# Performance work log

Hardware: AMD Instinct MI355X
Metric: run time of the kernel (lower is better)

The kernel has to match this reference:

```python
import math
import jax, jax.numpy as jnp
import numpy as np

B, T, C, H = 2, 2048, 1024, 16
D = C // H


def _slopes(n):
    def p2(m):
        start = 2 ** (-(2 ** -(math.log2(m) - 3)))
        return [start * start ** i for i in range(m)]
    if math.log2(n).is_integer():
        return p2(n)
    c = 2 ** math.floor(math.log2(n))
    return p2(c) + _slopes(2 * c)[0::2][: n - c]


def setup_inputs() -> dict:
    key = jax.random.key(0)
    ks = jax.random.split(key, 9)
    std = 0.02
    x = jax.random.normal(ks[0], (B, T, C), dtype=jnp.float32)
    Wq = std * jax.random.normal(ks[1], (C, C), dtype=jnp.float32)
    Wk = std * jax.random.normal(ks[2], (C, C), dtype=jnp.float32)
    Wv = std * jax.random.normal(ks[3], (C, C), dtype=jnp.float32)
    # fc_resid init: std 0.02/sqrt(num_layers)
    Wo = (std / math.sqrt(24.0)) * jax.random.normal(ks[4], (C, C), dtype=jnp.float32)
    bq = jnp.zeros((C,), jnp.float32)
    bk = jnp.zeros((C,), jnp.float32)
    bv = jnp.zeros((C,), jnp.float32)
    bo = jnp.zeros((C,), jnp.float32)
    return {"x": x, "Wq": Wq, "bq": bq, "Wk": Wk, "bk": bk,
            "Wv": Wv, "bv": bv, "Wo": Wo, "bo": bo}


def reference(x, Wq, bq, Wk, bk, Wv, bv, Wo, bo):
    # projections -> [B, T, H, D]
    q = (x @ Wq + bq).reshape(B, T, H, D)
    k = (x @ Wk + bk).reshape(B, T, H, D)
    v = (x @ Wv + bv).reshape(B, T, H, D)

    scale = 1.0 / math.sqrt(D)
    att = jnp.einsum("bqhd,bkhd->bhqk", q, k) * scale  # [B,H,T,T]

    slopes = jnp.asarray(_slopes(H), dtype=jnp.float32)  # [H]
    i = jnp.arange(T)
    rel = i[None, :] - i[None, :].T  # rel[i,j] = j - i
    causal = rel <= 0  # j <= i
    # alibi bias: -tril(i - j) = tril(j - i), scaled per head
    alibi = slopes[:, None, None] * jnp.where(causal, rel, 0).astype(jnp.float32)

    att = att + alibi[None]  # broadcast over batch
    att = jnp.where(causal[None, None], att, -jnp.inf)
    att = jax.nn.softmax(att, axis=-1)

    y = jnp.einsum("bhqk,bkhd->bqhd", att, v).reshape(B, T, C)
    return y @ Wo + bo  # dropout p=0 (eval) is identity
```

## Files before the change

### kernel.cpp

```cpp
#include <hip/hip_runtime.h>
#include <hip/hip_bf16.h>

typedef __bf16 bf16;
typedef __bf16 bf16x4 __attribute__((ext_vector_type(4)));
typedef __bf16 bf16x8 __attribute__((ext_vector_type(8)));
typedef float floatx4 __attribute__((ext_vector_type(4)));

#define B_ 2
#define T_ 2048
#define C_ 1024
#define H_ 16
#define D_ 64
#define M_ 4096
#define QK_LD 2048

__device__ __forceinline__ void load_lds16(const void* g, void* l) {
  __builtin_amdgcn_global_load_lds(
      (const __attribute__((address_space(1))) unsigned int*)g,
      (__attribute__((address_space(3))) unsigned int*)l, 16, 0, 0);
}

struct PrepArgs { const float* w[4]; bf16* wt[4]; const float* x; bf16* xb; };

__global__ __launch_bounds__(256)
void prep(PrepArgs p) {
  const int bid = blockIdx.x;
  if (bid < 4096) {
    __shared__ float tile[32][33];
    const int z = bid >> 10, xy = bid & 1023;
    const int bx = xy & 31, by = xy >> 5;
    const float* in = p.w[z];
    bf16* out = p.wt[z];
    int tx = threadIdx.x & 31, ty = threadIdx.x >> 5;
    int n0 = bx * 32, k0 = by * 32;
#pragma unroll
    for (int j = 0; j < 32; j += 8)
      tile[ty + j][tx] = in[(size_t)(k0 + ty + j) * C_ + n0 + tx];
    __syncthreads();
#pragma unroll
    for (int j = 0; j < 32; j += 8)
      out[(size_t)(n0 + ty + j) * C_ + k0 + tx] = (bf16)tile[tx][ty + j];
  } else {
    int i = ((bid - 4096) * 256 + threadIdx.x) * 8;
    float4 a = *(const float4*)(p.x + i);
    float4 b = *(const float4*)(p.x + i + 4);
    bf16x8 o;
    o[0] = (bf16)a.x; o[1] = (bf16)a.y; o[2] = (bf16)a.z; o[3] = (bf16)a.w;
    o[4] = (bf16)b.x; o[5] = (bf16)b.y; o[6] = (bf16)b.z; o[7] = (bf16)b.w;
    *(bf16x8*)(p.xb + i) = o;
  }
}

struct GQ {
  const bf16* A; const bf16* Bt;
  const float* bias[3];
  bf16* Cout; bf16* vt; int N; int K;
};

__global__ __launch_bounds__(256, 2)
void gemm128(GQ g) {
  __shared__ __align__(16) bf16 As[128 * 64];
  __shared__ __align__(16) bf16 Bs[128 * 64];
  const int tid = threadIdx.x;
  const int wave = tid >> 6, lane = tid & 63;
  const int quad = lane >> 4, l16 = lane & 15;
  const int m0 = blockIdx.y * 128, n0 = blockIdx.x * 128;
  const int wm = (wave >> 1) * 64, wn = (wave & 1) * 64;

  floatx4 acc[4][4] = {};

  int rA[4], cA[4];
#pragma unroll
  for (int t = 0; t < 4; ++t) {
    int pch = (wave * 4 + t) * 64 + lane;
    rA[t] = pch >> 3;
    cA[t] = (pch & 7) ^ (rA[t] & 7);
  }

  for (int k0 = 0; k0 < g.K; k0 += 64) {
    __syncthreads();
#pragma unroll
    for (int t = 0; t < 4; ++t) {
      load_lds16(g.A + (size_t)(m0 + rA[t]) * g.K + k0 + cA[t] * 8,
                 As + (wave * 4 + t) * 512);
      load_lds16(g.Bt + (size_t)(n0 + rA[t]) * g.K + k0 + cA[t] * 8,
                 Bs + (wave * 4 + t) * 512);
    }
    __builtin_amdgcn_s_waitcnt(0x0f70);
    __syncthreads();
#pragma unroll
    for (int s = 0; s < 2; ++s) {
      bf16x8 af[4], bfr[4];
#pragma unroll
      for (int i = 0; i < 4; ++i) {
        int mr = wm + i * 16 + l16;
        af[i] = *(const bf16x8*)(As + ((mr * 8) + ((s * 4 + quad) ^ (mr & 7))) * 8);
        int nr = wn + i * 16 + l16;
        bfr[i] = *(const bf16x8*)(Bs + ((nr * 8) + ((s * 4 + quad) ^ (nr & 7))) * 8);
      }
#pragma unroll
      for (int i = 0; i < 4; ++i)
#pragma unroll
        for (int j = 0; j < 4; ++j)
          acc[i][j] = __builtin_amdgcn_mfma_f32_16x16x32_bf16(af[i], bfr[j],
                                                              acc[i][j], 0, 0, 0);
    }
  }

  const bool vsplit = (n0 >= 2048);
#pragma unroll
  for (int j = 0; j < 4; ++j) {
    int col = n0 + wn + j * 16 + l16;
    const float* bp = g.bias[col >> 10];
    float bv = bp[col & 1023];
    if (vsplit) {
      int cv = col - 2048;
      bf16* dst0 = g.vt + ((size_t)((m0 >> 11) * 16 + (cv >> 6)) * 64 + (cv & 63)) * (size_t)T_
                   + (m0 & 2047) + wm + quad * 4;
#pragma unroll
      for (int i = 0; i < 4; ++i) {
        bf16x4 pk;
#pragma unroll
        for (int r = 0; r < 4; ++r) pk[r] = (bf16)(acc[i][j][r] + bv);
        *(bf16x4*)(dst0 + i * 16) = pk;
      }
    } else {
#pragma unroll
      for (int i = 0; i < 4; ++i) {
#pragma unroll
        for (int r = 0; r < 4; ++r) {
          int row = m0 + wm + i * 16 + quad * 4 + r;
          g.Cout[(size_t)row * g.N + col] = (bf16)(acc[i][j][r] + bv);
        }
      }
    }
  }
}

__global__ __launch_bounds__(256, 2)
void gemm_out(const bf16* __restrict__ A, const bf16* __restrict__ Bt,
              const float* __restrict__ bias, float* __restrict__ C) {
  __shared__ __align__(16) bf16 As[64 * 64];
  __shared__ __align__(16) bf16 Bs[128 * 64];
  const int tid = threadIdx.x;
  const int wave = tid >> 6, lane = tid & 63;
  const int quad = lane >> 4, l16 = lane & 15;
  const int m0 = blockIdx.y * 64, n0 = blockIdx.x * 128;
  const int wm = (wave >> 1) * 32, wn = (wave & 1) * 64;

  floatx4 acc[2][4] = {};

  int rA[2], cA[2], rB[4], cB[4];
#pragma unroll
  for (int t = 0; t < 2; ++t) {
    int p = t * 256 + tid;
    rA[t] = p >> 3; cA[t] = (p & 7) ^ (rA[t] & 7);
  }
#pragma unroll
  for (int t = 0; t < 4; ++t) {
    int p = t * 256 + tid;
    rB[t] = p >> 3; cB[t] = (p & 7) ^ (rB[t] & 7);
  }

  for (int k0 = 0; k0 < 1024; k0 += 64) {
    __syncthreads();
#pragma unroll
    for (int t = 0; t < 2; ++t)
      load_lds16(A + (size_t)(m0 + rA[t]) * 1024 + k0 + cA[t] * 8,
                 As + t * 2048 + wave * 512);
#pragma unroll
    for (int t = 0; t < 4; ++t)
      load_lds16(Bt + (size_t)(n0 + rB[t]) * 1024 + k0 + cB[t] * 8,
                 Bs + t * 2048 + wave * 512);
    __builtin_amdgcn_s_waitcnt(0x0f70);
    __syncthreads();
#pragma unroll
    for (int s = 0; s < 2; ++s) {
      bf16x8 af[2], bfr[4];
#pragma unroll
      for (int i = 0; i < 2; ++i) {
        int mr = wm + i * 16 + l16;
        af[i] = *(const bf16x8*)(As + ((mr * 8) + ((s * 4 + quad) ^ (mr & 7))) * 8);
      }
#pragma unroll
      for (int j = 0; j < 4; ++j) {
        int nr = wn + j * 16 + l16;
        bfr[j] = *(const bf16x8*)(Bs + ((nr * 8) + ((s * 4 + quad) ^ (nr & 7))) * 8);
      }
#pragma unroll
      for (int i = 0; i < 2; ++i)
#pragma unroll
        for (int j = 0; j < 4; ++j)
          acc[i][j] = __builtin_amdgcn_mfma_f32_16x16x32_bf16(af[i], bfr[j],
                                                              acc[i][j], 0, 0, 0);
    }
  }

#pragma unroll
  for (int j = 0; j < 4; ++j) {
    int col = n0 + wn + j * 16 + l16;
    float bv = bias[col];
#pragma unroll
    for (int i = 0; i < 2; ++i)
#pragma unroll
      for (int r = 0; r < 4; ++r) {
        int row = m0 + wm + i * 16 + quad * 4 + r;
        C[(size_t)row * 1024 + col] = acc[i][j][r] + bv;
      }
  }
}

__constant__ int yy_map[24] = {7, 8, 16, 9, 17, 6, 10, 18, 11, 19, 5, 12,
                               20, 13, 21, 4, 14, 22, 15, 23, 3, 2, 1, 0};

__global__ __launch_bounds__(512, 2)
void attn8(const bf16* __restrict__ qk, const bf16* __restrict__ vt,
           bf16* __restrict__ y, bf16* __restrict__ po, float* __restrict__ pl) {
  __shared__ __align__(16) bf16 smem[8192 + 8192 + 8 * 576];
  const int tid = threadIdx.x, wave = tid >> 6, lane = tid & 63;
  const int quad = lane >> 4, l16 = lane & 15;
  const int qs = wave >> 1, kh = wave & 1;
  const int bh = blockIdx.x, b = bh >> 4, h = bh & 15;
  const int yy = yy_map[blockIdx.y];
  int qb, kbeg, kcnt, seg;
  if (yy < 8)       { qb = yy;      kbeg = 0;      kcnt = 2 * qb + 2; seg = -1; }
  else if (yy < 16) { qb = 23 - yy; kbeg = 0;      kcnt = qb + 1;     seg = 0;  }
  else              { qb = 31 - yy; kbeg = qb + 1; kcnt = qb + 1;     seg = 1;  }

  const float L2E = 1.4426950408889634f;
  const float slope2 = exp2f(-0.5f * (float)(h + 1)) * L2E;
  const float scl2 = 0.125f * L2E;
  const float M0 = 14.0f;

  bf16x8 ones;
  {
    bf16 v1 = (l16 == 0) ? (bf16)1.0f : (bf16)0.0f;
#pragma unroll
    for (int j = 0; j < 8; ++j) ones[j] = v1;
  }

  const int rS = tid >> 3;
  const int cS = (tid & 7) ^ (rS & 7);
  const bf16* kbase = qk + (size_t)b * T_ * QK_LD + 1024 + h * 64;
  const bf16* vbase = vt + (size_t)bh * 64 * T_;

  bf16* Plw = smem + 16384 + wave * 576;
  const int q0 = qb * 128;
  const int w0 = q0 + qs * 32;

  bf16x8 qf[2][2];
  float rowoff[2][4];
#pragma unroll
  for (int qt = 0; qt < 2; ++qt) {
#pragma unroll
    for (int s = 0; s < 2; ++s)
      qf[qt][s] = *(const bf16x8*)(qk +
          (size_t)(b * T_ + w0 + qt * 16 + l16) * QK_LD + h * 64 + s * 32 + quad * 8);
#pragma unroll
    for (int r = 0; r < 4; ++r)
      rowoff[qt][r] = slope2 * (float)(w0 + qt * 16 + quad * 4 + r) + M0;
  }

  floatx4 o[2][5];
#pragma unroll
  for (int qt = 0; qt < 2; ++qt)
#pragma unroll
    for (int n = 0; n < 5; ++n) o[qt][n] = (floatx4)0.f;

  load_lds16(kbase + (size_t)(kbeg * 64 + rS) * QK_LD + cS * 8, smem + wave * 512);
  load_lds16(vbase + (size_t)rS * T_ + kbeg * 64 + cS * 8, smem + 8192 + wave * 512);
  __builtin_amdgcn_s_waitcnt(0x0f70);
  __syncthreads();

  for (int it = 0; it < kcnt; ++it) {
    const int kj0 = (kbeg + it) * 64;
    const int cur = it & 1;

    if (it + 1 < kcnt) {
      const int nk = kj0 + 64;
      load_lds16(kbase + (size_t)(nk + rS) * QK_LD + cS * 8,
                 smem + (cur ^ 1) * 4096 + wave * 512);
      load_lds16(vbase + (size_t)rS * T_ + nk + cS * 8,
                 smem + 8192 + (cur ^ 1) * 4096 + wave * 512);
    }

    const bf16* Klc = smem + cur * 4096;
    const bf16* Vlc = smem + 8192 + cur * 4096;
    bf16x8 kf[2][2], vf[4];
#pragma unroll
    for (int ss = 0; ss < 2; ++ss)
#pragma unroll
      for (int kt = 0; kt < 2; ++kt) {
        const int krow = kh * 32 + kt * 16 + l16;
        kf[ss][kt] = *(const bf16x8*)(Klc + krow * 64 +
                                      (((ss * 4 + quad) ^ (krow & 7)) * 8));
      }
#pragma unroll
    for (int nt = 0; nt < 4; ++nt) {
      const int drow = nt * 16 + l16;
      vf[nt] = *(const bf16x8*)(Vlc + drow * 64 +
                                (((kh * 4 + quad) ^ (drow & 7)) * 8));
    }

    float scol[2];
#pragma unroll
    for (int kt = 0; kt < 2; ++kt)
      scol[kt] = slope2 * (float)(kj0 + kh * 32 + kt * 16 + l16);

#pragma unroll
    for (int qt = 0; qt < 2; ++qt) {
      const int rb = w0 + qt * 16;
      floatx4 sa[2] = {};
#pragma unroll
      for (int ss = 0; ss < 2; ++ss)
#pragma unroll
        for (int kt = 0; kt < 2; ++kt)
          sa[kt] = __builtin_amdgcn_mfma_f32_16x16x32_bf16(qf[qt][ss], kf[ss][kt],
                                                           sa[kt], 0, 0, 0);

      if (kj0 + kh * 32 + 31 > rb) {
#pragma unroll
        for (int kt = 0; kt < 2; ++kt)
#pragma unroll
          for (int r = 0; r < 4; ++r) {
            const int row = rb + quad * 4 + r;
            float p = __builtin_amdgcn_exp2f(
                fmaf(sa[kt][r], scl2, scol[kt]) - rowoff[qt][r]);
            if (kj0 + kh * 32 + kt * 16 + l16 > row) p = 0.f;
            Plw[(quad * 4 + r) * 36 + kt * 16 + l16] = (bf16)p;
          }
      } else {
#pragma unroll
        for (int kt = 0; kt < 2; ++kt)
#pragma unroll
          for (int r = 0; r < 4; ++r)
            Plw[(quad * 4 + r) * 36 + kt * 16 + l16] = (bf16)__builtin_amdgcn_exp2f(
                fmaf(sa[kt][r], scl2, scol[kt]) - rowoff[qt][r]);
      }

      __builtin_amdgcn_s_waitcnt(0xc07f);

      bf16x8 pf = *(const bf16x8*)(Plw + l16 * 36 + quad * 8);
#pragma unroll
      for (int nt = 0; nt < 4; ++nt)
        o[qt][nt] = __builtin_amdgcn_mfma_f32_16x16x32_bf16(pf, vf[nt],
                                                            o[qt][nt], 0, 0, 0);
      o[qt][4] = __builtin_amdgcn_mfma_f32_16x16x32_bf16(pf, ones, o[qt][4], 0, 0, 0);
    }

    __builtin_amdgcn_s_waitcnt(0x0f70);
    __syncthreads();
  }

  float* Cb = (float*)smem;
  if (kh == 1) {
#pragma unroll
    for (int qt = 0; qt < 2; ++qt)
#pragma unroll
      for (int n = 0; n < 5; ++n)
        *(floatx4*)(Cb + (((qs * 2 + qt) * 5 + n) * 64 + lane) * 4) = o[qt][n];
  }
  __syncthreads();
  if (kh == 1) return;
#pragma unroll
  for (int qt = 0; qt < 2; ++qt)
#pragma unroll
    for (int n = 0; n < 5; ++n)
      o[qt][n] += *(const floatx4*)(Cb + (((qs * 2 + qt) * 5 + n) * 64 + lane) * 4);

  if (seg < 0) {
#pragma unroll
    for (int qt = 0; qt < 2; ++qt)
#pragma unroll
      for (int r = 0; r < 4; ++r) {
        float lsum = __shfl(o[qt][4][r], lane & 48);
        float inv = 1.f / lsum;
        const int row = w0 + qt * 16 + quad * 4 + r;
#pragma unroll
        for (int nt = 0; nt < 4; ++nt)
          y[(size_t)(b * T_ + row) * C_ + h * 64 + nt * 16 + l16] =
              (bf16)(o[qt][nt][r] * inv);
      }
  } else {
    const int pid = (bh * 8 + (qb - 8)) * 2 + seg;
    bf16* pob = po + (size_t)pid * 8192;
#pragma unroll
    for (int qt = 0; qt < 2; ++qt) {
#pragma unroll
      for (int half = 0; half < 2; ++half) {
        bf16x8 pk;
#pragma unroll
        for (int jj = 0; jj < 8; ++jj) {
          int j = half * 8 + jj;
          pk[jj] = (bf16)o[qt][j >> 2][j & 3];
        }
        *(bf16x8*)(pob + (qt * 2 + half) * 2048 + (qs * 64 + lane) * 8) = pk;
      }
#pragma unroll
      for (int r = 0; r < 4; ++r)
        if (l16 == 0)
          pl[pid * 128 + qs * 32 + qt * 16 + quad * 4 + r] = o[qt][4][r];
    }
  }
}

__global__ __launch_bounds__(256)
void combine(const bf16* __restrict__ po, const float* __restrict__ pl,
             bf16* __restrict__ y) {
  const int x = blockIdx.x;
  const int bh = x >> 3, qb = (x & 7) + 8;
  const int b = bh >> 4, h = bh & 15;
  const int pid0 = (bh * 8 + (qb - 8)) * 2;
  const bf16* p0 = po + (size_t)pid0 * 8192;
  const bf16* p1 = p0 + 8192;
  const int t = threadIdx.x;
  const int wave = t >> 6, quad = (t >> 4) & 3, l16 = t & 15;

  float linv[2][4];
#pragma unroll
  for (int qt = 0; qt < 2; ++qt)
#pragma unroll
    for (int r = 0; r < 4; ++r) {
      const int row = wave * 32 + qt * 16 + quad * 4 + r;
      linv[qt][r] = 1.f / (pl[pid0 * 128 + row] + pl[(pid0 + 1) * 128 + row]);
    }

#pragma unroll
  for (int qt = 0; qt < 2; ++qt)
#pragma unroll
    for (int half = 0; half < 2; ++half) {
      bf16x8 a = *(const bf16x8*)(p0 + (qt * 2 + half) * 2048 + t * 8);
      bf16x8 c = *(const bf16x8*)(p1 + (qt * 2 + half) * 2048 + t * 8);
#pragma unroll
      for (int jj = 0; jj < 8; ++jj) {
        int j = half * 8 + jj;
        const int nt = j >> 2, r = j & 3;
        const int row = wave * 32 + qt * 16 + quad * 4 + r;
        const int col = nt * 16 + l16;
        float v = ((float)a[jj] + (float)c[jj]) * linv[qt][r];
        y[(size_t)(b * T_ + qb * 128 + row) * C_ + h * 64 + col] = (bf16)v;
      }
    }
}

extern "C" void kernel_launch(void* const* d_in, const int* in_sizes, int n_in,
                              void* d_out, int out_size, void* d_ws, size_t ws_size,
                              hipStream_t stream) {
  const float* x  = (const float*)d_in[0];
  const float* Wq = (const float*)d_in[1];
  const float* bq = (const float*)d_in[2];
  const float* Wk = (const float*)d_in[3];
  const float* bk = (const float*)d_in[4];
  const float* Wv = (const float*)d_in[5];
  const float* bv = (const float*)d_in[6];
  const float* Wo = (const float*)d_in[7];
  const float* bo = (const float*)d_in[8];

  bf16* ws  = (bf16*)d_ws;
  bf16* WtQ = ws;
  bf16* WtK = WtQ + (size_t)C_ * C_;
  bf16* WtV = WtK + (size_t)C_ * C_;
  bf16* WtO = WtV + (size_t)C_ * C_;
  bf16* xb  = WtO + (size_t)C_ * C_;
  bf16* qkb = xb + (size_t)M_ * C_;
  bf16* vtb = qkb + (size_t)M_ * 2 * C_;
  bf16* yb  = vtb + (size_t)M_ * C_;
  bf16* pob = yb + (size_t)M_ * C_;
  float* plb = (float*)(pob + (size_t)512 * 8192);

  PrepArgs pp;
  pp.w[0] = Wq; pp.w[1] = Wk; pp.w[2] = Wv; pp.w[3] = Wo;
  pp.wt[0] = WtQ; pp.wt[1] = WtK; pp.wt[2] = WtV; pp.wt[3] = WtO;
  pp.x = x; pp.xb = xb;
  prep<<<dim3(4096 + M_ * C_ / (256 * 8)), 256, 0, stream>>>(pp);

  GQ gq;
  gq.A = xb; gq.Bt = WtQ;
  gq.bias[0] = bq; gq.bias[1] = bk; gq.bias[2] = bv;
  gq.Cout = qkb; gq.vt = vtb; gq.N = 2 * C_; gq.K = C_;
  gemm128<<<dim3(24, 32), 256, 0, stream>>>(gq);

  attn8<<<dim3(32, 24), 512, 0, stream>>>(qkb, vtb, yb, pob, plb);
  combine<<<dim3(32 * 8), 256, 0, stream>>>(pob, plb, yb);

  gemm_out<<<dim3(8, 64), 256, 0, stream>>>(yb, WtO, bo, (float*)d_out);
}
```

Before: 189.1 us.

## Compute transposed scores to keep P in registers and drop LDS round-trip

Attention now computes S^T = K·Q^T, so each lane's MFMA output can be fed directly as the B operand of 16x16x16 MFMAs for P·V. This removes the per-wave LDS staging of P, its wait, and the extra 'ones' MFMA used for row sums. Row sums are instead accumulated in registers and reduced with shuffles. Output stores become vectorized bf16x4 in both attn8 and combine. The trade is twice as many smaller-K MFMAs for P·V, plus a reworked V fragment layout.

```diff
diff --git a/kernel.cpp b/kernel.cpp
--- a/kernel.cpp
+++ b/kernel.cpp
@@ -5,6 +5,7 @@
 typedef __bf16 bf16x4 __attribute__((ext_vector_type(4)));
 typedef __bf16 bf16x8 __attribute__((ext_vector_type(8)));
 typedef float floatx4 __attribute__((ext_vector_type(4)));
+typedef short short4_ __attribute__((ext_vector_type(4)));
 
 #define B_ 2
 #define T_ 2048
@@ -18,6 +19,15 @@
   __builtin_amdgcn_global_load_lds(
       (const __attribute__((address_space(1))) unsigned int*)g,
       (__attribute__((address_space(3))) unsigned int*)l, 16, 0, 0);
+}
+
+__device__ __forceinline__ floatx4 mfma16(bf16x4 a, bf16x4 b, floatx4 c) {
+#if __has_builtin(__builtin_amdgcn_mfma_f32_16x16x16_bf16)
+  return __builtin_amdgcn_mfma_f32_16x16x16_bf16(a, b, c, 0, 0, 0);
+#else
+  return __builtin_amdgcn_mfma_f32_16x16x16bf16_1k(
+      __builtin_bit_cast(short4_, a), __builtin_bit_cast(short4_, b), c, 0, 0, 0);
+#endif
 }
 
 struct PrepArgs { const float* w[4]; bf16* wt[4]; const float* x; bf16* xb; };
@@ -216,7 +226,7 @@
 __global__ __launch_bounds__(512, 2)
 void attn8(const bf16* __restrict__ qk, const bf16* __restrict__ vt,
            bf16* __restrict__ y, bf16* __restrict__ po, float* __restrict__ pl) {
-  __shared__ __align__(16) bf16 smem[8192 + 8192 + 8 * 576];
+  __shared__ __align__(16) bf16 smem[17408];
   const int tid = threadIdx.x, wave = tid >> 6, lane = tid & 63;
   const int quad = lane >> 4, l16 = lane & 15;
   const int qs = wave >> 1, kh = wave & 1;
@@ -232,40 +242,39 @@
   const float scl2 = 0.125f * L2E;
   const float M0 = 14.0f;
 
-  bf16x8 ones;
-  {
-    bf16 v1 = (l16 == 0) ? (bf16)1.0f : (bf16)0.0f;
-#pragma unroll
-    for (int j = 0; j < 8; ++j) ones[j] = v1;
-  }
-
   const int rS = tid >> 3;
   const int cS = (tid & 7) ^ (rS & 7);
   const bf16* kbase = qk + (size_t)b * T_ * QK_LD + 1024 + h * 64;
   const bf16* vbase = vt + (size_t)bh * 64 * T_;
 
-  bf16* Plw = smem + 16384 + wave * 576;
   const int q0 = qb * 128;
   const int w0 = q0 + qs * 32;
 
   bf16x8 qf[2][2];
-  float rowoff[2][4];
-#pragma unroll
-  for (int qt = 0; qt < 2; ++qt) {
+#pragma unroll
+  for (int qt = 0; qt < 2; ++qt)
 #pragma unroll
     for (int s = 0; s < 2; ++s)
       qf[qt][s] = *(const bf16x8*)(qk +
           (size_t)(b * T_ + w0 + qt * 16 + l16) * QK_LD + h * 64 + s * 32 + quad * 8);
+
+  const int qi0 = w0 + l16;
+  float qoff[2];
+  qoff[0] = slope2 * (float)qi0 + M0;
+  qoff[1] = qoff[0] + slope2 * 16.0f;
+  float kc[2][4];
+#pragma unroll
+  for (int kt = 0; kt < 2; ++kt)
 #pragma unroll
     for (int r = 0; r < 4; ++r)
-      rowoff[qt][r] = slope2 * (float)(w0 + qt * 16 + quad * 4 + r) + M0;
-  }
-
-  floatx4 o[2][5];
+      kc[kt][r] = slope2 * (float)(kt * 16 + quad * 4 + r);
+
+  floatx4 o[2][4];
 #pragma unroll
   for (int qt = 0; qt < 2; ++qt)
 #pragma unroll
-    for (int n = 0; n < 5; ++n) o[qt][n] = (floatx4)0.f;
+    for (int n = 0; n < 4; ++n) o[qt][n] = (floatx4)0.f;
+  float lsum[2] = {0.f, 0.f};
 
   load_lds16(kbase + (size_t)(kbeg * 64 + rS) * QK_LD + cS * 8, smem + wave * 512);
   load_lds16(vbase + (size_t)rS * T_ + kbeg * 64 + cS * 8, smem + 8192 + wave * 512);
@@ -286,7 +295,8 @@
 
     const bf16* Klc = smem + cur * 4096;
     const bf16* Vlc = smem + 8192 + cur * 4096;
-    bf16x8 kf[2][2], vf[4];
+
+    bf16x8 kf[2][2];
 #pragma unroll
     for (int ss = 0; ss < 2; ++ss)
 #pragma unroll
@@ -295,57 +305,64 @@
         kf[ss][kt] = *(const bf16x8*)(Klc + krow * 64 +
                                       (((ss * 4 + quad) ^ (krow & 7)) * 8));
       }
+    bf16x4 vfr[4][2];
 #pragma unroll
     for (int nt = 0; nt < 4; ++nt) {
       const int drow = nt * 16 + l16;
-      vf[nt] = *(const bf16x8*)(Vlc + drow * 64 +
-                                (((kh * 4 + quad) ^ (drow & 7)) * 8));
-    }
-
-    float scol[2];
-#pragma unroll
-    for (int kt = 0; kt < 2; ++kt)
-      scol[kt] = slope2 * (float)(kj0 + kh * 32 + kt * 16 + l16);
+#pragma unroll
+      for (int kt = 0; kt < 2; ++kt) {
+        const int chunk = (kh * 4 + kt * 2 + (quad >> 1)) ^ (drow & 7);
+        vfr[nt][kt] = *(const bf16x4*)(Vlc + drow * 64 + chunk * 8 + (quad & 1) * 4);
+      }
+    }
+
+    const int kbi = kj0 + kh * 32;
+    const float kb = slope2 * (float)kbi;
 
 #pragma unroll
     for (int qt = 0; qt < 2; ++qt) {
       const int rb = w0 + qt * 16;
-      floatx4 sa[2] = {};
+      floatx4 st[2] = {};
 #pragma unroll
       for (int ss = 0; ss < 2; ++ss)
 #pragma unroll
         for (int kt = 0; kt < 2; ++kt)
-          sa[kt] = __builtin_amdgcn_mfma_f32_16x16x32_bf16(qf[qt][ss], kf[ss][kt],
-                                                           sa[kt], 0, 0, 0);
-
-      if (kj0 + kh * 32 + 31 > rb) {
+          st[kt] = __builtin_amdgcn_mfma_f32_16x16x32_bf16(kf[ss][kt], qf[qt][ss],
+                                                           st[kt], 0, 0, 0);
+
+      const float bb = kb - qoff[qt];
+      const int qi = qi0 + qt * 16;
+      bf16x4 pb[2];
+      if (kbi + 31 > rb) {
+#pragma unroll
+        for (int kt = 0; kt < 2; ++kt) {
+#pragma unroll
+          for (int r = 0; r < 4; ++r) {
+            float p = __builtin_amdgcn_exp2f(
+                fmaf(st[kt][r], scl2, bb + kc[kt][r]));
+            if (kbi + kt * 16 + quad * 4 + r > qi) p = 0.f;
+            lsum[qt] += p;
+            pb[kt][r] = (bf16)p;
+          }
+        }
+      } else {
+#pragma unroll
+        for (int kt = 0; kt < 2; ++kt) {
+#pragma unroll
+          for (int r = 0; r < 4; ++r) {
+            float p = __builtin_amdgcn_exp2f(
+                fmaf(st[kt][r], scl2, bb + kc[kt][r]));
+            lsum[qt] += p;
+            pb[kt][r] = (bf16)p;
+          }
+        }
+      }
+
+#pragma unroll
+      for (int nt = 0; nt < 4; ++nt)
 #pragma unroll
         for (int kt = 0; kt < 2; ++kt)
-#pragma unroll
-          for (int r = 0; r < 4; ++r) {
-            const int row = rb + quad * 4 + r;
-            float p = __builtin_amdgcn_exp2f(
-                fmaf(sa[kt][r], scl2, scol[kt]) - rowoff[qt][r]);
-            if (kj0 + kh * 32 + kt * 16 + l16 > row) p = 0.f;
-            Plw[(quad * 4 + r) * 36 + kt * 16 + l16] = (bf16)p;
-          }
-      } else {
-#pragma unroll
-        for (int kt = 0; kt < 2; ++kt)
-#pragma unroll
-          for (int r = 0; r < 4; ++r)
-            Plw[(quad * 4 + r) * 36 + kt * 16 + l16] = (bf16)__builtin_amdgcn_exp2f(
-                fmaf(sa[kt][r], scl2, scol[kt]) - rowoff[qt][r]);
-      }
-
-      __builtin_amdgcn_s_waitcnt(0xc07f);
-
-      bf16x8 pf = *(const bf16x8*)(Plw + l16 * 36 + quad * 8);
-#pragma unroll
-      for (int nt = 0; nt < 4; ++nt)
-        o[qt][nt] = __builtin_amdgcn_mfma_f32_16x16x32_bf16(pf, vf[nt],
-                                                            o[qt][nt], 0, 0, 0);
-      o[qt][4] = __builtin_amdgcn_mfma_f32_16x16x32_bf16(pf, ones, o[qt][4], 0, 0, 0);
+          o[qt][nt] = mfma16(vfr[nt][kt], pb[kt], o[qt][nt]);
     }
 
     __builtin_amdgcn_s_waitcnt(0x0f70);
@@ -355,32 +372,38 @@
   float* Cb = (float*)smem;
   if (kh == 1) {
 #pragma unroll
-    for (int qt = 0; qt < 2; ++qt)
-#pragma unroll
-      for (int n = 0; n < 5; ++n)
-        *(floatx4*)(Cb + (((qs * 2 + qt) * 5 + n) * 64 + lane) * 4) = o[qt][n];
+    for (int qt = 0; qt < 2; ++qt) {
+#pragma unroll
+      for (int n = 0; n < 4; ++n)
+        *(floatx4*)(Cb + (((qs * 2 + qt) * 4 + n) * 64 + lane) * 4) = o[qt][n];
+      Cb[8192 + (qs * 2 + qt) * 64 + lane] = lsum[qt];
+    }
   }
   __syncthreads();
   if (kh == 1) return;
 #pragma unroll
-  for (int qt = 0; qt < 2; ++qt)
-#pragma unroll
-    for (int n = 0; n < 5; ++n)
-      o[qt][n] += *(const floatx4*)(Cb + (((qs * 2 + qt) * 5 + n) * 64 + lane) * 4);
+  for (int qt = 0; qt < 2; ++qt) {
+#pragma unroll
+    for (int n = 0; n < 4; ++n)
+      o[qt][n] += *(const floatx4*)(Cb + (((qs * 2 + qt) * 4 + n) * 64 + lane) * 4);
+    lsum[qt] += Cb[8192 + (qs * 2 + qt) * 64 + lane];
+    lsum[qt] += __shfl_xor(lsum[qt], 16);
+    lsum[qt] += __shfl_xor(lsum[qt], 32);
+  }
 
   if (seg < 0) {
 #pragma unroll
-    for (int qt = 0; qt < 2; ++qt)
-#pragma unroll
-      for (int r = 0; r < 4; ++r) {
-        float lsum = __shfl(o[qt][4][r], lane & 48);
-        float inv = 1.f / lsum;
-        const int row = w0 + qt * 16 + quad * 4 + r;
-#pragma unroll
-        for (int nt = 0; nt < 4; ++nt)
-          y[(size_t)(b * T_ + row) * C_ + h * 64 + nt * 16 + l16] =
-              (bf16)(o[qt][nt][r] * inv);
-      }
+    for (int qt = 0; qt < 2; ++qt) {
+      const float inv = 1.f / lsum[qt];
+      bf16* yp = y + (size_t)(b * T_ + w0 + qt * 16 + l16) * C_ + h * 64 + quad * 4;
+#pragma unroll
+      for (int nt = 0; nt < 4; ++nt) {
+        bf16x4 pk;
+#pragma unroll
+        for (int r = 0; r < 4; ++r) pk[r] = (bf16)(o[qt][nt][r] * inv);
+        *(bf16x4*)(yp + nt * 16) = pk;
+      }
+    }
   } else {
     const int pid = (bh * 8 + (qb - 8)) * 2 + seg;
     bf16* pob = po + (size_t)pid * 8192;
@@ -390,16 +413,12 @@
       for (int half = 0; half < 2; ++half) {
         bf16x8 pk;
 #pragma unroll
-        for (int jj = 0; jj < 8; ++jj) {
-          int j = half * 8 + jj;
-          pk[jj] = (bf16)o[qt][j >> 2][j & 3];
-        }
+        for (int jj = 0; jj < 8; ++jj)
+          pk[jj] = (bf16)o[qt][half * 2 + (jj >> 2)][jj & 3];
         *(bf16x8*)(pob + (qt * 2 + half) * 2048 + (qs * 64 + lane) * 8) = pk;
       }
-#pragma unroll
-      for (int r = 0; r < 4; ++r)
-        if (l16 == 0)
-          pl[pid * 128 + qs * 32 + qt * 16 + quad * 4 + r] = o[qt][4][r];
+      if (quad == 0)
+        pl[pid * 128 + qs * 32 + qt * 16 + l16] = lsum[qt];
     }
   }
 }
@@ -414,16 +433,15 @@
   const bf16* p0 = po + (size_t)pid0 * 8192;
   const bf16* p1 = p0 + 8192;
   const int t = threadIdx.x;
-  const int wave = t >> 6, quad = (t >> 4) & 3, l16 = t & 15;
-
-  float linv[2][4];
-#pragma unroll
-  for (int qt = 0; qt < 2; ++qt)
-#pragma unroll
-    for (int r = 0; r < 4; ++r) {
-      const int row = wave * 32 + qt * 16 + quad * 4 + r;
-      linv[qt][r] = 1.f / (pl[pid0 * 128 + row] + pl[(pid0 + 1) * 128 + row]);
-    }
+  const int qs = t >> 6, quad = (t >> 4) & 3, l16 = t & 15;
+
+  float linv[2];
+  int row[2];
+#pragma unroll
+  for (int qt = 0; qt < 2; ++qt) {
+    row[qt] = qs * 32 + qt * 16 + l16;
+    linv[qt] = 1.f / (pl[pid0 * 128 + row[qt]] + pl[(pid0 + 1) * 128 + row[qt]]);
+  }
 
 #pragma unroll
   for (int qt = 0; qt < 2; ++qt)
@@ -432,13 +450,13 @@
       bf16x8 a = *(const bf16x8*)(p0 + (qt * 2 + half) * 2048 + t * 8);
       bf16x8 c = *(const bf16x8*)(p1 + (qt * 2 + half) * 2048 + t * 8);
 #pragma unroll
-      for (int jj = 0; jj < 8; ++jj) {
-        int j = half * 8 + jj;
-        const int nt = j >> 2, r = j & 3;
-        const int row = wave * 32 + qt * 16 + quad * 4 + r;
-        const int col = nt * 16 + l16;
-        float v = ((float)a[jj] + (float)c[jj]) * linv[qt][r];
-        y[(size_t)(b * T_ + qb * 128 + row) * C_ + h * 64 + col] = (bf16)v;
+      for (int g = 0; g < 2; ++g) {
+        bf16x4 outv;
+#pragma unroll
+        for (int r = 0; r < 4; ++r)
+          outv[r] = (bf16)(((float)a[g * 4 + r] + (float)c[g * 4 + r]) * linv[qt]);
+        const int col = (half * 2 + g) * 16 + quad * 4;
+        *(bf16x4*)(y + (size_t)(b * T_ + qb * 128 + row[qt]) * C_ + h * 64 + col) = outv;
       }
     }
 }
```

Result: faster. 179.6 us (-5.0%).
